# Performance work log

Measured on AMD Instinct MI355X. Metric: run time of the kernel, lower is better.

Reference implementation:

```python
import jax, jax.numpy as jnp
import numpy as np

N_HEADS = 12
NEG_BIG = 1e10  # matches torch source's -10000000000.0 masking constant


def setup_inputs() -> dict:
    key = jax.random.key(0)
    ks = jax.random.split(key, 5)
    nb, ns, nf = 4, 2048, 768
    return {
        "x": jax.random.normal(ks[0], (nb, ns, nf), dtype=jnp.float32),
        "Wqkv_w": jax.random.normal(ks[1], (3 * nf, nf), dtype=jnp.float32) * 0.02,
        "Wqkv_b": jax.random.normal(ks[2], (3 * nf,), dtype=jnp.float32) * 0.02,
        "Wproj_w": jax.random.normal(ks[3], (nf, nf), dtype=jnp.float32) * 0.02,
        "Wproj_b": jax.random.normal(ks[4], (nf,), dtype=jnp.float32) * 0.02,
    }


def reference(x, Wqkv_w, Wqkv_b, Wproj_w, Wproj_b):
    nb, ns, nf = x.shape
    hd = nf // N_HEADS
    qkv = x @ Wqkv_w.T + Wqkv_b            # [b, s, 3f]
    q = qkv[..., :nf]                       # source bug: k and v are taken from q
    q = q.reshape(nb, ns, N_HEADS, hd).transpose(0, 2, 1, 3)  # [b, h, s, d]
    k = q
    v = q
    w = jnp.einsum("bhqd,bhkd->bhqk", q, k) * (1.0 / jnp.sqrt(jnp.float32(hd)))
    mask = jnp.tril(jnp.ones((ns, ns), dtype=x.dtype))
    w = jax.nn.softmax(w * mask - NEG_BIG * (1.0 - mask), axis=-1)
    a = jnp.einsum("bhqk,bhkd->bhqd", w, v)
    a = a.transpose(0, 2, 1, 3).reshape(nb, ns, nf)
    return a @ Wproj_w.T + Wproj_b
```

## Files before the change

kernel.cpp:

```cpp
#include <hip/hip_runtime.h>
#include <hip/hip_bf16.h>

#define NF 768
#define NHEADS 12
#define NSEQ 2048
#define NX (8192 * 768)
#define NW (768 * 768)

#define QSC 0.42466090f

typedef __attribute__((__ext_vector_type__(8))) __bf16 bfrag;
typedef __attribute__((__ext_vector_type__(4))) float f32x4;
typedef __attribute__((__ext_vector_type__(16))) float f32x16;

static __device__ __forceinline__ unsigned short bfu(float f) {
    union { __hip_bfloat16 h; unsigned short u; } v;
    v.h = __float2bfloat16(f);
    return v.u;
}

static __device__ __forceinline__ int packrn(float lo, float hi) {
    union { __hip_bfloat162 h; int i; } u;
    u.h.x = __float2bfloat16(lo);
    u.h.y = __float2bfloat16(hi);
    return u.i;
}

static __device__ __forceinline__ float exp2a(float x) {
#if __has_builtin(__builtin_amdgcn_exp2f)
    return __builtin_amdgcn_exp2f(x);
#else
    return exp2f(x);
#endif
}

static __device__ __forceinline__ void plswap(int& a, int& b, int hi) {
#if __has_builtin(__builtin_amdgcn_permlane32_swap)
    auto r = __builtin_amdgcn_permlane32_swap((unsigned)a, (unsigned)b, false, false);
    a = (int)r[0]; b = (int)r[1];
#else
    int ta = __shfl_xor(b, 32), tb = __shfl_xor(a, 32);
    a = hi ? ta : a;
    b = hi ? b : tb;
#endif
}

static __device__ __forceinline__ float xhalf(float v, int hi) {
#if __has_builtin(__builtin_amdgcn_permlane32_swap)
    union { float f; unsigned u; } c; c.f = v;
    auto r = __builtin_amdgcn_permlane32_swap(c.u, c.u, false, false);
    union { unsigned u; float f; } d; d.u = hi ? r[0] : r[1];
    return d.f;
#else
    return __shfl_xor(v, 32);
#endif
}

static __device__ __forceinline__ void gload16(const unsigned short* g, unsigned short* l) {
#if __has_builtin(__builtin_amdgcn_global_load_lds)
    __builtin_amdgcn_global_load_lds(
        (const __attribute__((address_space(1))) void*)g,
        (__attribute__((address_space(3))) void*)l, 16, 0, 0);
#else
    *(uint4*)l = *(const uint4*)g;
#endif
}

__global__ __launch_bounds__(256) void preconv(const float* __restrict__ x,
                                               const float* __restrict__ W1,
                                               const float* __restrict__ W2,
                                               unsigned short* __restrict__ xb,
                                               unsigned short* __restrict__ W1b,
                                               unsigned short* __restrict__ W2b) {
    const size_t i = ((size_t)blockIdx.x * 256 + threadIdx.x) * 8;
    const float* src;
    unsigned short* dst;
    float scl = 1.0f;
    if (i < (size_t)NX) {
        src = x + i; dst = xb + i;
    } else if (i < (size_t)NX + NW) {
        const size_t j = i - NX;
        src = W1 + j; dst = W1b + j; scl = QSC;
    } else {
        const size_t j = i - NX - NW;
        src = W2 + j; dst = W2b + j;
    }
    float4 v0 = *(const float4*)(src);
    float4 v1 = *(const float4*)(src + 4);
    uint4 o;
    o.x = (unsigned)packrn(v0.x * scl, v0.y * scl);
    o.y = (unsigned)packrn(v0.z * scl, v0.w * scl);
    o.z = (unsigned)packrn(v1.x * scl, v1.y * scl);
    o.w = (unsigned)packrn(v1.z * scl, v1.w * scl);
    *(uint4*)dst = o;
}

__global__ __launch_bounds__(256) void gemm_qkv(const unsigned short* __restrict__ A,
                                                const unsigned short* __restrict__ B,
                                                const float* __restrict__ bias,
                                                unsigned short* __restrict__ Qo) {
    __shared__ unsigned short As[2 * 64 * 32];
    __shared__ unsigned short Bs[2 * 128 * 32];
    const int t    = threadIdx.x;
    const int bm   = blockIdx.x / 6, bn = blockIdx.x % 6;
    const int m0   = bm * 64, n0 = bn * 128;
    const int lane = t & 63;
    const int wid  = t >> 6;
    const int wm   = (wid >> 1) * 32, wn = (wid & 1) * 64;

    const unsigned short* ga  = A + (size_t)(m0 + (t >> 2)) * NF + (t & 3) * 8;
    const unsigned short* gb  = B + (size_t)(n0 + (t >> 2)) * NF + (t & 3) * 8;
    const unsigned short* gb2 = gb + (size_t)64 * NF;

    f32x4 acc[2][4];
#pragma unroll
    for (int i = 0; i < 2; i++)
#pragma unroll
        for (int j = 0; j < 4; j++) acc[i][j] = (f32x4)0.0f;

    for (int k0 = 0; k0 < NF; k0 += 64) {
        gload16(ga + k0,       &As[t * 8]);
        gload16(ga + k0 + 32,  &As[2048 + t * 8]);
        gload16(gb + k0,       &Bs[t * 8]);
        gload16(gb + k0 + 32,  &Bs[4096 + t * 8]);
        gload16(gb2 + k0,      &Bs[2048 + t * 8]);
        gload16(gb2 + k0 + 32, &Bs[4096 + 2048 + t * 8]);
        __syncthreads();

#pragma unroll
        for (int kk = 0; kk < 2; kk++) {
            bfrag af[2], bfr[4];
#pragma unroll
            for (int i = 0; i < 2; i++)
                af[i]  = *(const bfrag*)&As[kk*2048 + (wm + i*16 + (lane & 15)) * 32 + (lane >> 4) * 8];
#pragma unroll
            for (int j = 0; j < 4; j++)
                bfr[j] = *(const bfrag*)&Bs[kk*4096 + (wn + j*16 + (lane & 15)) * 32 + (lane >> 4) * 8];
#pragma unroll
            for (int i = 0; i < 2; i++)
#pragma unroll
                for (int j = 0; j < 4; j++)
                    acc[i][j] = __builtin_amdgcn_mfma_f32_16x16x32_bf16(af[i], bfr[j], acc[i][j], 0, 0, 0);
        }
        __syncthreads();
    }

#pragma unroll
    for (int j = 0; j < 4; j++) {
        const int col = n0 + wn + j*16 + (lane & 15);
        const float bq = QSC * bias[col];
#pragma unroll
        for (int i = 0; i < 2; i++) {
            const int rbase = m0 + wm + i*16 + ((lane >> 4) << 2);
#pragma unroll
            for (int r = 0; r < 4; r++)
                Qo[(size_t)(rbase + r) * NF + col] = bfu(acc[i][j][r] + bq);
        }
    }
}

__global__ __launch_bounds__(256) void gemm_proj(const unsigned short* __restrict__ A,
                                                 const unsigned short* __restrict__ B,
                                                 const float* __restrict__ bias,
                                                 float* __restrict__ out) {
    __shared__ unsigned short As[2 * 64 * 32];
    __shared__ unsigned short Bs[2 * 128 * 32];
    const int t    = threadIdx.x;
    const int bm   = blockIdx.x / 6, bn = blockIdx.x % 6;
    const int m0   = bm * 64, n0 = bn * 128;
    const int lane = t & 63;
    const int wid  = t >> 6;
    const int wm   = (wid >> 1) * 32, wn = (wid & 1) * 64;

    const unsigned short* ga  = A + (size_t)(m0 + (t >> 2)) * NF + (t & 3) * 8;
    const unsigned short* gb  = B + (size_t)(n0 + (t >> 2)) * NF + (t & 3) * 8;
    const unsigned short* gb2 = gb + (size_t)64 * NF;

    f32x4 acc[2][4];
#pragma unroll
    for (int i = 0; i < 2; i++)
#pragma unroll
        for (int j = 0; j < 4; j++) acc[i][j] = (f32x4)0.0f;

    for (int k0 = 0; k0 < NF; k0 += 64) {
        gload16(ga + k0,       &As[t * 8]);
        gload16(ga + k0 + 32,  &As[2048 + t * 8]);
        gload16(gb + k0,       &Bs[t * 8]);
        gload16(gb + k0 + 32,  &Bs[4096 + t * 8]);
        gload16(gb2 + k0,      &Bs[2048 + t * 8]);
        gload16(gb2 + k0 + 32, &Bs[4096 + 2048 + t * 8]);
        __syncthreads();

#pragma unroll
        for (int kk = 0; kk < 2; kk++) {
            bfrag af[2], bfr[4];
#pragma unroll
            for (int i = 0; i < 2; i++)
                af[i]  = *(const bfrag*)&As[kk*2048 + (wm + i*16 + (lane & 15)) * 32 + (lane >> 4) * 8];
#pragma unroll
            for (int j = 0; j < 4; j++)
                bfr[j] = *(const bfrag*)&Bs[kk*4096 + (wn + j*16 + (lane & 15)) * 32 + (lane >> 4) * 8];
#pragma unroll
            for (int i = 0; i < 2; i++)
#pragma unroll
                for (int j = 0; j < 4; j++)
                    acc[i][j] = __builtin_amdgcn_mfma_f32_16x16x32_bf16(af[i], bfr[j], acc[i][j], 0, 0, 0);
        }
        __syncthreads();
    }

#pragma unroll
    for (int j = 0; j < 4; j++) {
        const int col = n0 + wn + j*16 + (lane & 15);
        const float bvv = bias[col];
#pragma unroll
        for (int i = 0; i < 2; i++) {
            const int rbase = m0 + wm + i*16 + ((lane >> 4) << 2);
#pragma unroll
            for (int r = 0; r < 4; r++)
                out[(size_t)(rbase + r) * NF + col] = acc[i][j][r] + bvv;
        }
    }
}

__global__ __launch_bounds__(256, 1) void attn(const unsigned short* __restrict__ Q,
                                               unsigned short* __restrict__ O) {
    const int pair = blockIdx.x;
    const int bh   = blockIdx.y;
    const int b    = bh / NHEADS, h = bh % NHEADS;
    const unsigned short* base = Q + (size_t)b * NSEQ * NF + h * 64;
    unsigned short*       ob   = O + (size_t)b * NSEQ * NF + h * 64;

    const int t    = threadIdx.x;
    const int w    = t >> 6;
    const int qsub = w & 1;
    const int kh   = w >> 1;
    const int l31  = t & 31;
    const int hi   = (t >> 5) & 1;
    const int sw   = l31 & 7;
    const int svw  = (l31 & 7) ^ ((l31 >> 2) & 7);

    __shared__ float smem[4096];
    unsigned short* Ks = (unsigned short*)smem;
    unsigned short* Vt = (unsigned short*)smem + 4096;
    float* mO = smem;
    __shared__ float ml[2][2][32];

    for (int half = 0; half < 2; half++) {
        const int qt  = half ? (31 - pair) : pair;
        const int wq0 = qt * 64 + qsub * 32;
        const int qg  = wq0 + l31;

        bfrag qf[4];
#pragma unroll
        for (int c16 = 0; c16 < 4; c16++)
            qf[c16] = *(const bfrag*)(base + (size_t)qg * NF + c16*16 + hi*8);

        f32x16 o[2];
#pragma unroll
        for (int fd = 0; fd < 2; fd++)
#pragma unroll
            for (int r = 0; r < 16; r++) o[fd][r] = 0.0f;
        float m_ = -3.0e38f, l_ = 0.0f;

        const int ktend = qt + 1;
        for (int kt = 0; kt < ktend; kt++) {
            const int k0 = kt * 64;

            if (t < 128) {
                const int r = t >> 1, c = t & 1;
                const unsigned short* kg = base + (size_t)(k0 + r) * NF + c * 32;
#pragma unroll
                for (int i = 0; i < 4; i++) {
                    uint4 v = *(const uint4*)(kg + i * 8);
                    const int u = (4 * c + i) ^ (r & 7);
                    *(uint4*)&Ks[r * 64 + u * 8] = v;
                }
            } else {
                const int tt = t - 128;
                const int p = tt & 15, g2 = tt >> 4;
                const unsigned short* vg = base + (size_t)(k0 + 8 * g2) * NF + 4 * p;
                uint2 ld[8];
#pragma unroll
                for (int i = 0; i < 8; i++) ld[i] = *(const uint2*)(vg + (size_t)i * NF);
#pragma unroll
                for (int j = 0; j < 4; j++) {
                    const int d = 4 * p + j;
                    union { unsigned short hh[8]; uint4 q; } wv;
#pragma unroll
                    for (int i = 0; i < 8; i++) wv.hh[i] = ((const unsigned short*)&ld[i])[j];
                    const int u = g2 ^ (d & 7) ^ ((d >> 2) & 7);
                    *(uint4*)&Vt[d * 64 + u * 8] = wv.q;
                }
            }
            __syncthreads();

            if (k0 + 32 * kh <= wq0 + 31) {
                f32x16 s;
#pragma unroll
                for (int r = 0; r < 16; r++) s[r] = 0.0f;
                __builtin_amdgcn_s_setprio(1);
#pragma unroll
                for (int c16 = 0; c16 < 4; c16++) {
                    bfrag ka = *(const bfrag*)&Ks[(kh*32 + l31)*64 + (((2*c16 + hi) ^ sw) * 8)];
                    s = __builtin_amdgcn_mfma_f32_32x32x16_bf16(ka, qf[c16], s, 0, 0, 0);
                }
                __builtin_amdgcn_s_setprio(0);

                if (k0 + 32*kh + 31 > wq0) {
#pragma unroll
                    for (int r = 0; r < 16; r++) {
                        const int kp = k0 + 32*kh + (r & 3) + 8*(r >> 2) + 4*hi;
                        if (kp > qg) s[r] = -1.0e30f;
                    }
                }

                float mx = -3.0e38f;
#pragma unroll
                for (int r = 0; r < 16; r++) mx = fmaxf(mx, s[r]);
                mx = fmaxf(mx, xhalf(mx, hi));

                const bool nogrow = __all(mx <= m_ + 8.0f);
                const float mn = nogrow ? m_ : fmaxf(m_, mx);
                float rs = 0.0f;
#pragma unroll
                for (int r = 0; r < 16; r++) {
                    const float p = exp2a(s[r] - mn);
                    s[r] = p;
                    rs += p;
                }
                rs += xhalf(rs, hi);
                if (nogrow) {
                    l_ += rs;
                } else {
                    const float sc = exp2a(m_ - mn);
                    l_ = l_ * sc + rs;
                    m_ = mn;
#pragma unroll
                    for (int fd = 0; fd < 2; fd++)
#pragma unroll
                        for (int r = 0; r < 16; r++) o[fd][r] *= sc;
                }

                int wv_[4][2];
#pragma unroll
                for (int f = 0; f < 4; f++)
#pragma unroll
                    for (int rr = 0; rr < 2; rr++)
                        wv_[f][rr] = packrn(s[4*f + 2*rr], s[4*f + 2*rr + 1]);
#pragma unroll
                for (int c = 0; c < 2; c++) {
                    int x0 = wv_[2*c][0], y0 = wv_[2*c+1][0];
                    plswap(x0, y0, hi);
                    int x1 = wv_[2*c][1], y1 = wv_[2*c+1][1];
                    plswap(x1, y1, hi);
                    union { int d[4]; bfrag f; } pf;
                    pf.d[0] = x0; pf.d[1] = x1; pf.d[2] = y0; pf.d[3] = y1;
                    const int ck = kh*2 + c;
                    __builtin_amdgcn_s_setprio(1);
#pragma unroll
                    for (int fd = 0; fd < 2; fd++) {
                        bfrag va = *(const bfrag*)&Vt[(fd*32 + l31)*64 + (((2*ck + hi) ^ svw) * 8)];
                        o[fd] = __builtin_amdgcn_mfma_f32_32x32x16_bf16(va, pf.f, o[fd], 0, 0, 0);
                    }
                    __builtin_amdgcn_s_setprio(0);
                }
            }
            __syncthreads();
        }

        if (kh == 1) {
#pragma unroll
            for (int fd = 0; fd < 2; fd++)
#pragma unroll
                for (int r = 0; r < 16; r++) {
                    const int d = 32*fd + 8*(r >> 2) + 4*hi + (r & 3);
                    mO[qsub * 2048 + d * 32 + l31] = o[fd][r];
                }
            if (hi == 0) { ml[qsub][0][l31] = m_; ml[qsub][1][l31] = l_; }
        }
        __syncthreads();

        if (kh == 0) {
            const float mB = ml[qsub][0][l31];
            const float lB = ml[qsub][1][l31];
            const float mm = fmaxf(m_, mB);
            const float aa = exp2a(m_ - mm);
            const float bb = exp2a(mB - mm);
            const float ll = l_ * aa + lB * bb;
            const float inv = 1.0f / (ll * QSC);
#pragma unroll
            for (int fd = 0; fd < 2; fd++) {
                float ov[16];
#pragma unroll
                for (int r = 0; r < 16; r++) {
                    const int d = 32*fd + 8*(r >> 2) + 4*hi + (r & 3);
                    ov[r] = (o[fd][r] * aa + mO[qsub * 2048 + d * 32 + l31] * bb) * inv;
                }
#pragma unroll
                for (int f = 0; f < 4; f++) {
                    const int d0 = fd*32 + 8*f + 4*hi;
                    uint2 pr;
                    pr.x = (unsigned)packrn(ov[4*f+0], ov[4*f+1]);
                    pr.y = (unsigned)packrn(ov[4*f+2], ov[4*f+3]);
                    *(uint2*)(ob + (size_t)qg * NF + d0) = pr;
                }
            }
        }
        __syncthreads();
    }
}

extern "C" void kernel_launch(void* const* d_in, const int* in_sizes, int n_in,
                              void* d_out, int out_size, void* d_ws, size_t ws_size,
                              hipStream_t stream) {
    const float* x    = (const float*)d_in[0];
    const float* Wqkv = (const float*)d_in[1];
    const float* bqkv = (const float*)d_in[2];
    const float* Wp   = (const float*)d_in[3];
    const float* bp   = (const float*)d_in[4];
    float* out        = (float*)d_out;

    unsigned short* Qws = (unsigned short*)d_ws;
    unsigned short* Aws = Qws + (size_t)NX;
    unsigned short* xb  = Aws + (size_t)NX;
    unsigned short* W1b = xb + (size_t)NX;
    unsigned short* W2b = W1b + (size_t)NW;

    preconv<<<3648, 256, 0, stream>>>(x, Wqkv, Wp, xb, W1b, W2b);
    gemm_qkv<<<768, 256, 0, stream>>>(xb, W1b, bqkv, Qws);
    attn<<<dim3(16, 48), 256, 0, stream>>>(Qws, Aws);
    gemm_proj<<<768, 256, 0, stream>>>(Aws, W2b, bp, out);
}
```

Before: 120.4 us.

## Double attention block to 512 threads splitting key tiles across two wave groups

The attention kernel now runs 8 waves per block instead of 4. Each iteration stages two 64-key tiles into separate shared-memory buffers, and the two wave groups each process one tile (kpar). A two-level merge of the partial softmax states (m, l, O) happens at the end. This adds more parallelism per block and halves the number of barrier-separated iterations, at the cost of doubled shared memory, extra merge passes and barriers, and possible idle waves on the diagonal tile when the key count is odd.

```diff
diff --git a/kernel.cpp b/kernel.cpp
--- a/kernel.cpp
+++ b/kernel.cpp
@@ -223,7 +223,7 @@
     }
 }
 
-__global__ __launch_bounds__(256, 1) void attn(const unsigned short* __restrict__ Q,
+__global__ __launch_bounds__(512, 1) void attn(const unsigned short* __restrict__ Q,
                                                unsigned short* __restrict__ O) {
     const int pair = blockIdx.x;
     const int bh   = blockIdx.y;
@@ -234,17 +234,17 @@
     const int t    = threadIdx.x;
     const int w    = t >> 6;
     const int qsub = w & 1;
-    const int kh   = w >> 1;
+    const int kh   = (w >> 1) & 1;
+    const int kpar = w >> 2;
     const int l31  = t & 31;
     const int hi   = (t >> 5) & 1;
     const int sw   = l31 & 7;
     const int svw  = (l31 & 7) ^ ((l31 >> 2) & 7);
 
-    __shared__ float smem[4096];
-    unsigned short* Ks = (unsigned short*)smem;
-    unsigned short* Vt = (unsigned short*)smem + 4096;
-    float* mO = smem;
-    __shared__ float ml[2][2][32];
+    __shared__ float smem[8192];
+    unsigned short* us = (unsigned short*)smem;
+    __shared__ float mlA[2][2][2][32];
+    __shared__ float mlB[2][2][32];
 
     for (int half = 0; half < 2; half++) {
         const int qt  = half ? (31 - pair) : pair;
@@ -263,23 +263,26 @@
             for (int r = 0; r < 16; r++) o[fd][r] = 0.0f;
         float m_ = -3.0e38f, l_ = 0.0f;
 
-        const int ktend = qt + 1;
-        for (int kt = 0; kt < ktend; kt++) {
-            const int k0 = kt * 64;
-
-            if (t < 128) {
-                const int r = t >> 1, c = t & 1;
-                const unsigned short* kg = base + (size_t)(k0 + r) * NF + c * 32;
+        const int neps = (qt + 2) >> 1;
+        for (int ep = 0; ep < neps; ep++) {
+            const int k0 = ep * 128;
+            const int tt = t & 127;
+            const int spar = (t >> 7) & 1;
+
+            if (t < 256) {
+                const int r = tt >> 1, c = tt & 1;
+                const unsigned short* kg = base + (size_t)(k0 + spar*64 + r) * NF + c * 32;
+                unsigned short* Kb = us + spar * 4096;
 #pragma unroll
                 for (int i = 0; i < 4; i++) {
                     uint4 v = *(const uint4*)(kg + i * 8);
                     const int u = (4 * c + i) ^ (r & 7);
-                    *(uint4*)&Ks[r * 64 + u * 8] = v;
+                    *(uint4*)&Kb[r * 64 + u * 8] = v;
                 }
             } else {
-                const int tt = t - 128;
                 const int p = tt & 15, g2 = tt >> 4;
-                const unsigned short* vg = base + (size_t)(k0 + 8 * g2) * NF + 4 * p;
+                const unsigned short* vg = base + (size_t)(k0 + spar*64 + 8 * g2) * NF + 4 * p;
+                unsigned short* Vb = us + 8192 + spar * 4096;
                 uint2 ld[8];
 #pragma unroll
                 for (int i = 0; i < 8; i++) ld[i] = *(const uint2*)(vg + (size_t)i * NF);
@@ -290,27 +293,31 @@
 #pragma unroll
                     for (int i = 0; i < 8; i++) wv.hh[i] = ((const unsigned short*)&ld[i])[j];
                     const int u = g2 ^ (d & 7) ^ ((d >> 2) & 7);
-                    *(uint4*)&Vt[d * 64 + u * 8] = wv.q;
+                    *(uint4*)&Vb[d * 64 + u * 8] = wv.q;
                 }
             }
             __syncthreads();
 
-            if (k0 + 32 * kh <= wq0 + 31) {
+            const int k0b = k0 + 64 * kpar + 32 * kh;
+            if (k0b <= wq0 + 31) {
+                const unsigned short* ksb = us + kpar * 4096;
+                const unsigned short* vtb = us + 8192 + kpar * 4096;
+
                 f32x16 s;
 #pragma unroll
                 for (int r = 0; r < 16; r++) s[r] = 0.0f;
                 __builtin_amdgcn_s_setprio(1);
 #pragma unroll
                 for (int c16 = 0; c16 < 4; c16++) {
-                    bfrag ka = *(const bfrag*)&Ks[(kh*32 + l31)*64 + (((2*c16 + hi) ^ sw) * 8)];
+                    bfrag ka = *(const bfrag*)&ksb[(kh*32 + l31)*64 + (((2*c16 + hi) ^ sw) * 8)];
                     s = __builtin_amdgcn_mfma_f32_32x32x16_bf16(ka, qf[c16], s, 0, 0, 0);
                 }
                 __builtin_amdgcn_s_setprio(0);
 
-                if (k0 + 32*kh + 31 > wq0) {
+                if (k0b + 31 > wq0) {
 #pragma unroll
                     for (int r = 0; r < 16; r++) {
-                        const int kp = k0 + 32*kh + (r & 3) + 8*(r >> 2) + 4*hi;
+                        const int kp = k0b + (r & 3) + 8*(r >> 2) + 4*hi;
                         if (kp > qg) s[r] = -1.0e30f;
                     }
                 }
@@ -360,7 +367,7 @@
                     __builtin_amdgcn_s_setprio(1);
 #pragma unroll
                     for (int fd = 0; fd < 2; fd++) {
-                        bfrag va = *(const bfrag*)&Vt[(fd*32 + l31)*64 + (((2*ck + hi) ^ svw) * 8)];
+                        bfrag va = *(const bfrag*)&vtb[(fd*32 + l31)*64 + (((2*ck + hi) ^ svw) * 8)];
                         o[fd] = __builtin_amdgcn_mfma_f32_32x32x16_bf16(va, pf.f, o[fd], 0, 0, 0);
                     }
                     __builtin_amdgcn_s_setprio(0);
@@ -375,15 +382,45 @@
 #pragma unroll
                 for (int r = 0; r < 16; r++) {
                     const int d = 32*fd + 8*(r >> 2) + 4*hi + (r & 3);
-                    mO[qsub * 2048 + d * 32 + l31] = o[fd][r];
-                }
-            if (hi == 0) { ml[qsub][0][l31] = m_; ml[qsub][1][l31] = l_; }
+                    smem[(qsub*2 + kpar) * 2048 + d * 32 + l31] = o[fd][r];
+                }
+            if (hi == 0) { mlA[qsub][kpar][0][l31] = m_; mlA[qsub][kpar][1][l31] = l_; }
         }
         __syncthreads();
 
         if (kh == 0) {
-            const float mB = ml[qsub][0][l31];
-            const float lB = ml[qsub][1][l31];
+            const float mB = mlA[qsub][kpar][0][l31];
+            const float lB = mlA[qsub][kpar][1][l31];
+            const float mm = fmaxf(m_, mB);
+            const float aa = exp2a(m_ - mm);
+            const float bb = exp2a(mB - mm);
+            l_ = l_ * aa + lB * bb;
+#pragma unroll
+            for (int fd = 0; fd < 2; fd++)
+#pragma unroll
+                for (int r = 0; r < 16; r++) {
+                    const int d = 32*fd + 8*(r >> 2) + 4*hi + (r & 3);
+                    o[fd][r] = o[fd][r] * aa + smem[(qsub*2 + kpar) * 2048 + d * 32 + l31] * bb;
+                }
+            m_ = mm;
+        }
+        __syncthreads();
+
+        if (kh == 0 && kpar == 1) {
+#pragma unroll
+            for (int fd = 0; fd < 2; fd++)
+#pragma unroll
+                for (int r = 0; r < 16; r++) {
+                    const int d = 32*fd + 8*(r >> 2) + 4*hi + (r & 3);
+                    smem[qsub * 2048 + d * 32 + l31] = o[fd][r];
+                }
+            if (hi == 0) { mlB[qsub][0][l31] = m_; mlB[qsub][1][l31] = l_; }
+        }
+        __syncthreads();
+
+        if (kh == 0 && kpar == 0) {
+            const float mB = mlB[qsub][0][l31];
+            const float lB = mlB[qsub][1][l31];
             const float mm = fmaxf(m_, mB);
             const float aa = exp2a(m_ - mm);
             const float bb = exp2a(mB - mm);
@@ -395,7 +432,7 @@
 #pragma unroll
                 for (int r = 0; r < 16; r++) {
                     const int d = 32*fd + 8*(r >> 2) + 4*hi + (r & 3);
-                    ov[r] = (o[fd][r] * aa + mO[qsub * 2048 + d * 32 + l31] * bb) * inv;
+                    ov[r] = (o[fd][r] * aa + smem[qsub * 2048 + d * 32 + l31] * bb) * inv;
                 }
 #pragma unroll
                 for (int f = 0; f < 4; f++) {
@@ -429,6 +466,6 @@
 
     preconv<<<3648, 256, 0, stream>>>(x, Wqkv, Wp, xb, W1b, W2b);
     gemm_qkv<<<768, 256, 0, stream>>>(xb, W1b, bqkv, Qws);
-    attn<<<dim3(16, 48), 256, 0, stream>>>(Qws, Aws);
+    attn<<<dim3(16, 48), 512, 0, stream>>>(Qws, Aws);
     gemm_proj<<<768, 256, 0, stream>>>(Aws, W2b, bp, out);
 }
```

Result: slower. 131.1 us (+8.8%).
